# Performance work log

Hardware: AMD Instinct MI355X
Metric: run time of the kernel (lower is better)

The kernel has to match this reference:

```python
import jax, jax.numpy as jnp
import numpy as np


def setup_inputs() -> dict:
    key = jax.random.key(0)
    k1, k2, k3, k4 = jax.random.split(key, 4)
    B, n_env, in_ch, out_ch, code_ch, modes1, L = 16, 8, 32, 32, 16, 64, 8192
    scale = 1.0 / (in_ch * out_ch)
    return {
        "x": jax.random.normal(k1, (B, n_env * in_ch, L), dtype=jnp.float32),
        "codes": jax.random.normal(k2, (n_env, code_ch), dtype=jnp.float32),
        "com_weights": scale * jax.random.uniform(k3, (in_ch, out_ch, modes1, 2), dtype=jnp.float32),
        "code_weights": scale * jax.random.uniform(k4, (code_ch * in_ch, out_ch, modes1, 2), dtype=jnp.float32),
        "filter_weights": -3.0 * jnp.ones((modes1,), dtype=jnp.float32),
    }


def _as_complex(w):
    return w[..., 0] + 1j * w[..., 1]


def reference(x, codes, com_weights, code_weights, filter_weights):
    B, C, L = x.shape
    n_env, code_ch = codes.shape
    in_ch = C // n_env
    out_ch = com_weights.shape[1]
    modes1 = com_weights.shape[2]
    n_freq = L // 2 + 1

    # FFT and reshape to [B, e, i, freq]
    x_ft = jnp.fft.rfft(x).reshape(B, n_env, in_ch, n_freq)
    xm = x_ft[..., :modes1]  # mode truncation

    cw = _as_complex(com_weights)  # [i, o, m]
    codew = _as_complex(code_weights.reshape(code_ch, in_ch, out_ch, modes1, 2))  # [c,i,o,m]
    env_w = jnp.einsum('ec,ciom->eiom', codes.astype(codew.dtype), codew)

    # hardsigmoid(filter_weights): clip(x/6 + 0.5, 0, 1)
    lam = jnp.clip(filter_weights / 6.0 + 0.5, 0.0, 1.0)  # [m]

    out_m = (lam * jnp.einsum('beim,iom->beom', xm, cw)
             + (1.0 - lam) * jnp.einsum('beim,eiom->beom', xm, env_w))  # [B,e,o,m]

    # zero-pad back to full spectrum then inverse FFT
    out_ft = jnp.zeros((B, n_env, out_ch, n_freq), dtype=out_m.dtype)
    out_ft = out_ft.at[..., :modes1].set(out_m)
    out_ft = out_ft.reshape(B, n_env * out_ch, n_freq)
    return jnp.fft.irfft(out_ft, n=L)
```

## Files before the change

### kernel.cpp

```cpp
#include <hip/hip_runtime.h>
#include <hip/hip_bf16.h>
#include <math.h>
#include <stdint.h>

typedef __bf16 bf16_t;
typedef __bf16 bf16x4v __attribute__((ext_vector_type(4)));
typedef __bf16 bf16x8 __attribute__((ext_vector_type(8)));
typedef float  f32x4  __attribute__((ext_vector_type(4)));

#define L_LEN 8192
#define MODES 64
#define NCOMP 128
#define M_ROWS 4096

__global__ void gen_b1(bf16_t* __restrict__ B1) {
  int id = blockIdx.x * 256 + threadIdx.x;
  int l = id >> 6;
  int k = id & 63;
  float fr = (float)((l * k) & (L_LEN - 1)) * (1.0f / 8192.0f);
  float c = __builtin_amdgcn_cosf(fr);
  float s = __builtin_amdgcn_sinf(fr);
  B1[l * NCOMP + k]         = (bf16_t)c;
  B1[l * NCOMP + MODES + k] = (bf16_t)(-s);
}

__global__ void gen_b1t(bf16_t* __restrict__ B1t) {
  int id = blockIdx.x * 256 + threadIdx.x;
  int k  = id >> 11;
  int l0 = (id & 2047) * 4;
  bf16x4v cv, sv;
#pragma unroll
  for (int j = 0; j < 4; ++j) {
    float fr = (float)(((l0 + j) * k) & (L_LEN - 1)) * (1.0f / 8192.0f);
    cv[j] = (bf16_t)__builtin_amdgcn_cosf(fr);
    sv[j] = (bf16_t)(-__builtin_amdgcn_sinf(fr));
  }
  *(bf16x4v*)(B1t + (size_t)k * L_LEN + l0)        = cv;
  *(bf16x4v*)(B1t + (size_t)(k + 64) * L_LEN + l0) = sv;
}

__global__ void wmix(const float* __restrict__ codes, const float* __restrict__ comw,
                     const float* __restrict__ codew, const float* __restrict__ fw,
                     float* __restrict__ W) {
  int id = blockIdx.x * 256 + threadIdx.x;
  int k = id & 63;
  int o = (id >> 6) & 31;
  int i = (id >> 11) & 31;
  int e = id >> 16;
  float lam = fminf(fmaxf(fw[k] * (1.0f / 6.0f) + 0.5f, 0.0f), 1.0f);
  float are = 0.f, aim = 0.f;
#pragma unroll
  for (int c = 0; c < 16; ++c) {
    float cd = codes[e * 16 + c];
    const float* p = codew + ((((c * 32 + i) * 32 + o) * 64 + k) << 1);
    are += cd * p[0];
    aim += cd * p[1];
  }
  const float* q = comw + (((i * 32 + o) * 64 + k) << 1);
  float wre = lam * q[0] + (1.f - lam) * are;
  float wim = lam * q[1] + (1.f - lam) * aim;
  float* dst = W + ((((e * 32 + i) * 32 + o) * 64 + k) << 1);
  dst[0] = wre;
  dst[1] = wim;
}

__global__ __launch_bounds__(256) void stage1(const float* __restrict__ x,
                                              const bf16_t* __restrict__ B1t,
                                              float* __restrict__ X) {
  const int t = threadIdx.x;
  const int lane = t & 63;
  const int w = t >> 6;
  const int wm = w >> 1, wn = w & 1;
  const int mt = blockIdx.x;
  const int sp = blockIdx.y;
  const int lq = lane >> 4, l15 = lane & 15;
  const int mbase = mt * 64 + wm * 32;

  f32x4 acc[2][4];
#pragma unroll
  for (int a = 0; a < 2; ++a)
#pragma unroll
    for (int b = 0; b < 4; ++b) acc[a][b] = (f32x4){0.f, 0.f, 0.f, 0.f};

  const float*  xr0 = x + (size_t)(mbase + l15) * L_LEN + lq * 8;
  const bf16_t* bp0 = B1t + (size_t)(wn * 64 + l15) * L_LEN + lq * 8;

#pragma unroll 2
  for (int ks = 0; ks < 16; ++ks) {
    const int k0 = sp * 512 + ks * 32;
    bf16x8 a[2];
#pragma unroll
    for (int mf = 0; mf < 2; ++mf) {
      const float4* ap = (const float4*)(xr0 + (size_t)mf * 16 * L_LEN + k0);
      float4 p0 = ap[0], p1 = ap[1];
      a[mf] = (bf16x8){(bf16_t)p0.x, (bf16_t)p0.y, (bf16_t)p0.z, (bf16_t)p0.w,
                       (bf16_t)p1.x, (bf16_t)p1.y, (bf16_t)p1.z, (bf16_t)p1.w};
    }
    bf16x8 b[4];
#pragma unroll
    for (int nf = 0; nf < 4; ++nf)
      b[nf] = *(const bf16x8*)(bp0 + (size_t)nf * 16 * L_LEN + k0);
#pragma unroll
    for (int mf = 0; mf < 2; ++mf)
#pragma unroll
      for (int nf = 0; nf < 4; ++nf)
        acc[mf][nf] = __builtin_amdgcn_mfma_f32_16x16x32_bf16(a[mf], b[nf], acc[mf][nf], 0, 0, 0);
  }

#pragma unroll
  for (int mf = 0; mf < 2; ++mf)
#pragma unroll
    for (int nf = 0; nf < 4; ++nf) {
      int n = wn * 64 + nf * 16 + l15;
#pragma unroll
      for (int rg = 0; rg < 4; ++rg) {
        int m = mbase + mf * 16 + lq * 4 + rg;
        atomicAdd(X + (size_t)m * NCOMP + n, acc[mf][nf][rg]);
      }
    }
}

__global__ __launch_bounds__(256) void mixk(const float* __restrict__ X,
                                            const float* __restrict__ W,
                                            bf16_t* __restrict__ A2) {
  __shared__ float Xs[32 * 128];
  const int t = threadIdx.x;
  const int be = blockIdx.x;
  const int e = be & 7;
#pragma unroll
  for (int j = 0; j < 16; ++j) {
    int idx = t + 256 * j;
    Xs[idx] = X[(size_t)be * 4096 + idx];
  }
  __syncthreads();
  const int k = t & 63;
  const int olo = t >> 6;
  float yre[8], yim[8];
#pragma unroll
  for (int j = 0; j < 8; ++j) { yre[j] = 0.f; yim[j] = 0.f; }
  for (int i = 0; i < 32; ++i) {
    float xr = Xs[i * 128 + k];
    float xi = Xs[i * 128 + 64 + k];
    const float* wp = W + ((((e * 32 + i) * 32 + olo * 8) * 64 + k) << 1);
#pragma unroll
    for (int j = 0; j < 8; ++j) {
      float2 wv = *(const float2*)(wp + j * 128);
      yre[j] += xr * wv.x - xi * wv.y;
      yim[j] += xr * wv.y + xi * wv.x;
    }
  }
  float sc = (k == 0) ? (1.0f / 8192.0f) : (2.0f / 8192.0f);
#pragma unroll
  for (int j = 0; j < 8; ++j) {
    int m = be * 32 + olo * 8 + j;
    A2[m * NCOMP + k]         = (bf16_t)(yre[j] * sc);
    A2[m * NCOMP + MODES + k] = (bf16_t)(yim[j] * sc);
  }
}

__global__ __launch_bounds__(256) void stage2(const bf16_t* __restrict__ A2,
                                              const bf16_t* __restrict__ B1,
                                              float* __restrict__ out) {
  const int t = threadIdx.x;
  const int lane = t & 63;
  const int w = t >> 6;
  const int wm = w >> 1, wl = w & 1;
  const int lt = blockIdx.x, mt = blockIdx.y;
  const int lq = lane >> 4, l15 = lane & 15;

  f32x4 acc[4][4];
#pragma unroll
  for (int a = 0; a < 4; ++a)
#pragma unroll
    for (int b = 0; b < 4; ++b) acc[a][b] = (f32x4){0.f, 0.f, 0.f, 0.f};

  const bf16_t* ap0 = A2 + (size_t)(mt * 128 + wm * 64 + l15) * NCOMP + lq * 8;
  const bf16_t* bp0 = B1 + (size_t)(lt * 128 + wl * 64 + l15) * NCOMP + lq * 8;

#pragma unroll 2
  for (int s = 0; s < 4; ++s) {
    bf16x8 a[4], b[4];
#pragma unroll
    for (int mf = 0; mf < 4; ++mf)
      a[mf] = *(const bf16x8*)(ap0 + mf * 16 * NCOMP + s * 32);
#pragma unroll
    for (int nf = 0; nf < 4; ++nf)
      b[nf] = *(const bf16x8*)(bp0 + nf * 16 * NCOMP + s * 32);
#pragma unroll
    for (int mf = 0; mf < 4; ++mf)
#pragma unroll
      for (int nf = 0; nf < 4; ++nf)
        acc[mf][nf] = __builtin_amdgcn_mfma_f32_16x16x32_bf16(a[mf], b[nf], acc[mf][nf], 0, 0, 0);
  }

#pragma unroll
  for (int mf = 0; mf < 4; ++mf)
#pragma unroll
    for (int nf = 0; nf < 4; ++nf) {
      int m = mt * 128 + wm * 64 + mf * 16 + lq * 4;
      int l = lt * 128 + wl * 64 + nf * 16 + l15;
      float* op = out + (size_t)m * L_LEN + l;
#pragma unroll
      for (int rg = 0; rg < 4; ++rg) op[(size_t)rg * L_LEN] = acc[mf][nf][rg];
    }
}

extern "C" void kernel_launch(void* const* d_in, const int* in_sizes, int n_in,
                              void* d_out, int out_size, void* d_ws, size_t ws_size,
                              hipStream_t stream) {
  const float* x     = (const float*)d_in[0];
  const float* codes = (const float*)d_in[1];
  const float* comw  = (const float*)d_in[2];
  const float* codew = (const float*)d_in[3];
  const float* fw    = (const float*)d_in[4];
  float* out = (float*)d_out;
  char* ws = (char*)d_ws;
  bf16_t* B1t = (bf16_t*)(ws);
  bf16_t* B1  = (bf16_t*)(ws + (size_t)(2u << 20));
  float*  X   = (float*) (ws + (size_t)(4u << 20));
  float*  W   = (float*) (ws + (size_t)(6u << 20));
  bf16_t* A2  = (bf16_t*)(ws + (size_t)(10u << 20));

  gen_b1 <<<2048, 256, 0, stream>>>(B1);
  gen_b1t<<<512, 256, 0, stream>>>(B1t);
  wmix<<<2048, 256, 0, stream>>>(codes, comw, codew, fw, W);
  hipMemsetAsync(X, 0, (size_t)M_ROWS * NCOMP * sizeof(float), stream);
  stage1<<<dim3(64, 16), 256, 0, stream>>>(x, B1t, X);
  mixk<<<128, 256, 0, stream>>>(X, W, A2);
  stage2<<<dim3(64, 32), 256, 0, stream>>>(A2, B1, out);
}
```

Before: 336.4 us.

## Stage x tiles in LDS, split-K partials without atomics, coalesce stage2 stores

Stage1 now loads x rows with coalesced float4 reads, converts them to bf16 in shared memory, and writes per-split partial sums to separate buffers instead of using atomicAdd. This removes the memset and the atomic traffic. mixk reduces the eight partials on load. Stage2 changes its tile shape and routes its output through shared memory so each row is written as contiguous float4 stores rather than strided scalar ones. The cost is extra workspace and partial-buffer traffic, plus more synchronisation.

```diff
diff --git a/kernel.cpp b/kernel.cpp
--- a/kernel.cpp
+++ b/kernel.cpp
@@ -12,6 +12,7 @@
 #define MODES 64
 #define NCOMP 128
 #define M_ROWS 4096
+#define NSPLIT 8
 
 __global__ void gen_b1(bf16_t* __restrict__ B1) {
   int id = blockIdx.x * 256 + threadIdx.x;
@@ -57,70 +58,73 @@
     aim += cd * p[1];
   }
   const float* q = comw + (((i * 32 + o) * 64 + k) << 1);
-  float wre = lam * q[0] + (1.f - lam) * are;
-  float wim = lam * q[1] + (1.f - lam) * aim;
   float* dst = W + ((((e * 32 + i) * 32 + o) * 64 + k) << 1);
-  dst[0] = wre;
-  dst[1] = wim;
+  dst[0] = lam * q[0] + (1.f - lam) * are;
+  dst[1] = lam * q[1] + (1.f - lam) * aim;
 }
 
 __global__ __launch_bounds__(256) void stage1(const float* __restrict__ x,
                                               const bf16_t* __restrict__ B1t,
-                                              float* __restrict__ X) {
+                                              float* __restrict__ Xp) {
+  __shared__ bf16_t Al[32 * 264];
   const int t = threadIdx.x;
   const int lane = t & 63;
   const int w = t >> 6;
-  const int wm = w >> 1, wn = w & 1;
-  const int mt = blockIdx.x;
-  const int sp = blockIdx.y;
   const int lq = lane >> 4, l15 = lane & 15;
-  const int mbase = mt * 64 + wm * 32;
-
-  f32x4 acc[2][4];
+  const int mt = blockIdx.x, sp = blockIdx.y;
+  const int mbase = mt * 32;
+  const int wv = t >> 6, ln = t & 63;
+
+  f32x4 acc[2][2];
 #pragma unroll
   for (int a = 0; a < 2; ++a)
 #pragma unroll
-    for (int b = 0; b < 4; ++b) acc[a][b] = (f32x4){0.f, 0.f, 0.f, 0.f};
-
-  const float*  xr0 = x + (size_t)(mbase + l15) * L_LEN + lq * 8;
-  const bf16_t* bp0 = B1t + (size_t)(wn * 64 + l15) * L_LEN + lq * 8;
-
-#pragma unroll 2
-  for (int ks = 0; ks < 16; ++ks) {
-    const int k0 = sp * 512 + ks * 32;
-    bf16x8 a[2];
-#pragma unroll
-    for (int mf = 0; mf < 2; ++mf) {
-      const float4* ap = (const float4*)(xr0 + (size_t)mf * 16 * L_LEN + k0);
-      float4 p0 = ap[0], p1 = ap[1];
-      a[mf] = (bf16x8){(bf16_t)p0.x, (bf16_t)p0.y, (bf16_t)p0.z, (bf16_t)p0.w,
-                       (bf16_t)p1.x, (bf16_t)p1.y, (bf16_t)p1.z, (bf16_t)p1.w};
-    }
-    bf16x8 b[4];
-#pragma unroll
-    for (int nf = 0; nf < 4; ++nf)
-      b[nf] = *(const bf16x8*)(bp0 + (size_t)nf * 16 * L_LEN + k0);
-#pragma unroll
-    for (int mf = 0; mf < 2; ++mf)
-#pragma unroll
-      for (int nf = 0; nf < 4; ++nf)
-        acc[mf][nf] = __builtin_amdgcn_mfma_f32_16x16x32_bf16(a[mf], b[nf], acc[mf][nf], 0, 0, 0);
-  }
-
+    for (int b = 0; b < 2; ++b) acc[a][b] = (f32x4){0.f, 0.f, 0.f, 0.f};
+
+  for (int ch = 0; ch < 4; ++ch) {
+    const int k0 = sp * 1024 + ch * 256;
+    float4 xv[8];
+#pragma unroll
+    for (int rr = 0; rr < 8; ++rr)
+      xv[rr] = *(const float4*)(x + (size_t)(mbase + rr * 4 + wv) * L_LEN + k0 + ln * 4);
+    __syncthreads();
+#pragma unroll
+    for (int rr = 0; rr < 8; ++rr) {
+      bf16x4v v = {(bf16_t)xv[rr].x, (bf16_t)xv[rr].y, (bf16_t)xv[rr].z, (bf16_t)xv[rr].w};
+      *(bf16x4v*)(Al + (rr * 4 + wv) * 264 + ln * 4) = v;
+    }
+    __syncthreads();
+#pragma unroll
+    for (int s = 0; s < 8; ++s) {
+      bf16x8 a[2], b[2];
+#pragma unroll
+      for (int mf = 0; mf < 2; ++mf)
+        a[mf] = *(const bf16x8*)(Al + (mf * 16 + l15) * 264 + s * 32 + lq * 8);
+#pragma unroll
+      for (int nf = 0; nf < 2; ++nf)
+        b[nf] = *(const bf16x8*)(B1t + (size_t)(w * 32 + nf * 16 + l15) * L_LEN + k0 + s * 32 + lq * 8);
+#pragma unroll
+      for (int mf = 0; mf < 2; ++mf)
+#pragma unroll
+        for (int nf = 0; nf < 2; ++nf)
+          acc[mf][nf] = __builtin_amdgcn_mfma_f32_16x16x32_bf16(a[mf], b[nf], acc[mf][nf], 0, 0, 0);
+    }
+  }
+  float* xout = Xp + ((size_t)sp << 19);
 #pragma unroll
   for (int mf = 0; mf < 2; ++mf)
 #pragma unroll
-    for (int nf = 0; nf < 4; ++nf) {
-      int n = wn * 64 + nf * 16 + l15;
+    for (int nf = 0; nf < 2; ++nf) {
+      int n = w * 32 + nf * 16 + l15;
 #pragma unroll
       for (int rg = 0; rg < 4; ++rg) {
         int m = mbase + mf * 16 + lq * 4 + rg;
-        atomicAdd(X + (size_t)m * NCOMP + n, acc[mf][nf][rg]);
+        xout[(size_t)m * NCOMP + n] = acc[mf][nf][rg];
       }
     }
 }
 
-__global__ __launch_bounds__(256) void mixk(const float* __restrict__ X,
+__global__ __launch_bounds__(256) void mixk(const float* __restrict__ Xp,
                                             const float* __restrict__ W,
                                             bf16_t* __restrict__ A2) {
   __shared__ float Xs[32 * 128];
@@ -128,9 +132,12 @@
   const int be = blockIdx.x;
   const int e = be & 7;
 #pragma unroll
-  for (int j = 0; j < 16; ++j) {
-    int idx = t + 256 * j;
-    Xs[idx] = X[(size_t)be * 4096 + idx];
+  for (int j = 0; j < 4; ++j) {
+    f32x4 a = (f32x4){0.f, 0.f, 0.f, 0.f};
+#pragma unroll
+    for (int sp = 0; sp < NSPLIT; ++sp)
+      a += *(const f32x4*)(Xp + ((size_t)sp << 19) + (size_t)be * 4096 + (t + j * 256) * 4);
+    *(f32x4*)(Xs + (t + j * 256) * 4) = a;
   }
   __syncthreads();
   const int k = t & 63;
@@ -161,12 +168,13 @@
 __global__ __launch_bounds__(256) void stage2(const bf16_t* __restrict__ A2,
                                               const bf16_t* __restrict__ B1,
                                               float* __restrict__ out) {
+  __shared__ float Es[32 * 260];
   const int t = threadIdx.x;
   const int lane = t & 63;
   const int w = t >> 6;
-  const int wm = w >> 1, wl = w & 1;
   const int lt = blockIdx.x, mt = blockIdx.y;
   const int lq = lane >> 4, l15 = lane & 15;
+  const int ln = t & 63;
 
   f32x4 acc[4][4];
 #pragma unroll
@@ -174,8 +182,8 @@
 #pragma unroll
     for (int b = 0; b < 4; ++b) acc[a][b] = (f32x4){0.f, 0.f, 0.f, 0.f};
 
-  const bf16_t* ap0 = A2 + (size_t)(mt * 128 + wm * 64 + l15) * NCOMP + lq * 8;
-  const bf16_t* bp0 = B1 + (size_t)(lt * 128 + wl * 64 + l15) * NCOMP + lq * 8;
+  const bf16_t* ap0 = A2 + (size_t)(mt * 64 + l15) * NCOMP + lq * 8;
+  const bf16_t* bp0 = B1 + (size_t)(lt * 256 + w * 64 + l15) * NCOMP + lq * 8;
 
 #pragma unroll 2
   for (int s = 0; s < 4; ++s) {
@@ -194,15 +202,25 @@
   }
 
 #pragma unroll
-  for (int mf = 0; mf < 4; ++mf)
-#pragma unroll
-    for (int nf = 0; nf < 4; ++nf) {
-      int m = mt * 128 + wm * 64 + mf * 16 + lq * 4;
-      int l = lt * 128 + wl * 64 + nf * 16 + l15;
-      float* op = out + (size_t)m * L_LEN + l;
-#pragma unroll
-      for (int rg = 0; rg < 4; ++rg) op[(size_t)rg * L_LEN] = acc[mf][nf][rg];
-    }
+  for (int h = 0; h < 2; ++h) {
+    __syncthreads();
+#pragma unroll
+    for (int mm = 0; mm < 2; ++mm) {
+      int mf = 2 * h + mm;
+#pragma unroll
+      for (int nf = 0; nf < 4; ++nf)
+#pragma unroll
+        for (int rg = 0; rg < 4; ++rg)
+          Es[(mm * 16 + lq * 4 + rg) * 260 + w * 64 + nf * 16 + l15] = acc[mf][nf][rg];
+    }
+    __syncthreads();
+#pragma unroll
+    for (int rr = 0; rr < 8; ++rr) {
+      int row = rr * 4 + w;
+      f32x4 v = *(const f32x4*)(Es + row * 260 + ln * 4);
+      *(f32x4*)(out + (size_t)(mt * 64 + h * 32 + row) * L_LEN + lt * 256 + ln * 4) = v;
+    }
+  }
 }
 
 extern "C" void kernel_launch(void* const* d_in, const int* in_sizes, int n_in,
@@ -217,15 +235,14 @@
   char* ws = (char*)d_ws;
   bf16_t* B1t = (bf16_t*)(ws);
   bf16_t* B1  = (bf16_t*)(ws + (size_t)(2u << 20));
-  float*  X   = (float*) (ws + (size_t)(4u << 20));
-  float*  W   = (float*) (ws + (size_t)(6u << 20));
-  bf16_t* A2  = (bf16_t*)(ws + (size_t)(10u << 20));
+  float*  Xp  = (float*) (ws + (size_t)(4u << 20));
+  float*  W   = (float*) (ws + (size_t)(20u << 20));
+  bf16_t* A2  = (bf16_t*)(ws + (size_t)(24u << 20));
 
   gen_b1 <<<2048, 256, 0, stream>>>(B1);
   gen_b1t<<<512, 256, 0, stream>>>(B1t);
   wmix<<<2048, 256, 0, stream>>>(codes, comw, codew, fw, W);
-  hipMemsetAsync(X, 0, (size_t)M_ROWS * NCOMP * sizeof(float), stream);
-  stage1<<<dim3(64, 16), 256, 0, stream>>>(x, B1t, X);
-  mixk<<<128, 256, 0, stream>>>(X, W, A2);
-  stage2<<<dim3(64, 32), 256, 0, stream>>>(A2, B1, out);
-}
+  stage1<<<dim3(128, NSPLIT), 256, 0, stream>>>(x, B1t, Xp);
+  mixk<<<128, 256, 0, stream>>>(Xp, W, A2);
+  stage2<<<dim3(32, 64), 256, 0, stream>>>(A2, B1, out);
+}
```

Result: faster. 327.3 us (-2.7%).
